# Kernel tuning notes

Hardware: AMD Instinct MI355X
Metric: run time of the kernel (lower is better)

Reference implementation:

```python
import jax, jax.numpy as jnp
from jax import lax
import numpy as np
import math

INPUT_DIM = 64
HIDDEN_DIM = 512
SEQ_LEN = 256
BATCH = 512
PRED_LEN = 24
NUM_TARGETS = 1


def setup_inputs() -> dict:
    key = jax.random.key(0)
    ks = jax.random.split(key, 10)
    stdv = 1.0 / math.sqrt(HIDDEN_DIM)
    u = lambda k, shape: jax.random.uniform(k, shape, jnp.float32, -stdv, stdv)
    return {
        "x": jax.random.normal(ks[0], (BATCH, SEQ_LEN, INPUT_DIM), jnp.float32),
        "Wa": u(ks[1], (INPUT_DIM, INPUT_DIM)),
        "Ua": u(ks[2], (2 * HIDDEN_DIM, INPUT_DIM)),
        "ba": jnp.zeros((INPUT_DIM,), jnp.float32),
        "Va": u(ks[3], (INPUT_DIM, INPUT_DIM)),
        "W_ih": u(ks[4], (4 * HIDDEN_DIM, INPUT_DIM)),
        "W_hh": u(ks[5], (4 * HIDDEN_DIM, HIDDEN_DIM)),
        "b_ih": u(ks[6], (4 * HIDDEN_DIM,)),
        "b_hh": u(ks[7], (4 * HIDDEN_DIM,)),
        "fc_w": u(ks[8], (PRED_LEN * NUM_TARGETS, HIDDEN_DIM)),
        "fc_b": u(ks[9], (PRED_LEN * NUM_TARGETS,)),
    }


def reference(x, Wa, Ua, ba, Va, W_ih, W_hh, b_ih, b_hh, fc_w, fc_b):
    B, S, D = x.shape
    H = W_hh.shape[1]

    def step(carry, x_t):
        h, c = carry  # [B,H] each
        # attention gate over input features
        hc = jnp.concatenate([h, c], axis=1)  # [B,2H]
        a_t = jnp.tanh(x_t @ Wa + hc @ Ua + ba) @ Va  # [B,D]
        alpha_t = jax.nn.softmax(a_t, axis=1)
        x_att = alpha_t * x_t
        # torch.nn.LSTMCell: gates in order i, f, g, o
        gates = x_att @ W_ih.T + h @ W_hh.T + b_ih + b_hh  # [B,4H]
        i, f, g, o = jnp.split(gates, 4, axis=1)
        c_new = jax.nn.sigmoid(f) * c + jax.nn.sigmoid(i) * jnp.tanh(g)
        h_new = jax.nn.sigmoid(o) * jnp.tanh(c_new)
        return (h_new, c_new), None

    h0 = jnp.zeros((B, H), x.dtype)
    c0 = jnp.zeros((B, H), x.dtype)
    (h_T, _), _ = lax.scan(step, (h0, c0), jnp.swapaxes(x, 0, 1))  # scan over seq
    y = h_T @ fc_w.T + fc_b  # [B, pred_len*num_targets]
    return y.reshape(B, PRED_LEN, NUM_TARGETS)
```

## Files before the change

### kernel.cpp

```cpp
#include <hip/hip_runtime.h>
#include <math.h>

#define B 512
#define S 256
#define D 64
#define H 512
#define BH (B*H)

typedef __attribute__((ext_vector_type(8))) short short8;
typedef __attribute__((ext_vector_type(4))) float f32x4;

__device__ inline unsigned short f2bf(float v) {
    unsigned int u = __float_as_uint(v);
    unsigned int r = (u + 0x7fffu + ((u >> 16) & 1u)) >> 16;
    return (unsigned short)r;
}
__device__ inline float bf2f(unsigned short b) {
    return __uint_as_float(((unsigned int)b) << 16);
}

__global__ __launch_bounds__(256) void init_zero(
    float* __restrict__ h32, float* __restrict__ c32,
    unsigned short* __restrict__ hHi, unsigned short* __restrict__ hLo)
{
    int i = blockIdx.x * blockDim.x + threadIdx.x;
    if (i < BH) {
        h32[i] = 0.f;
        c32[i] = 0.f;
        hHi[i] = 0;
        hLo[i] = 0;
    }
}

__global__ __launch_bounds__(256) void prep_weights(
    const float* __restrict__ Whh, const float* __restrict__ Wih,
    unsigned short* __restrict__ wswz)
{
    const int jt = blockIdx.x;
    const int kb = blockIdx.y;
    const int t = threadIdx.x;
    const int jj = t >> 3;
    const int kk8 = t & 7;
    const int jg = jt*32 + jj;
    const int u = jg >> 2, q = jg & 3;
    const int Wrow = q*H + u;

    const float* src = (kb < 8) ? (Whh + (size_t)Wrow*H + kb*64 + kk8*8)
                                : (Wih + (size_t)Wrow*D + kk8*8);
    float v[8];
    *(float4*)&v[0] = *(const float4*)(src);
    *(float4*)&v[4] = *(const float4*)(src + 4);

    unsigned short hi[8], lo[8];
    #pragma unroll
    for (int e = 0; e < 8; ++e) {
        hi[e] = f2bf(v[e]);
        lo[e] = f2bf(v[e] - bf2f(hi[e]));
    }
    const int ks = kk8 >> 2, cg = kk8 & 3;
    const size_t slab = (size_t)(jt*9 + kb) * 4096;
    const size_t oH = slab + (size_t)(0*2048 + ks*1024 + cg*256 + jj*8);
    const size_t oL = slab + (size_t)(1*2048 + ks*1024 + cg*256 + jj*8);
    *(short8*)(wswz + oH) = *(const short8*)hi;
    *(short8*)(wswz + oL) = *(const short8*)lo;
}

__global__ __launch_bounds__(256) void attn_kernel(
    const float* __restrict__ x, const float* __restrict__ Wa,
    const float* __restrict__ Ua, const float* __restrict__ ba,
    const float* __restrict__ Va,
    const float* __restrict__ h32, const float* __restrict__ c32,
    unsigned short* __restrict__ xHi, unsigned short* __restrict__ xLo, int t)
{
    const int d = threadIdx.x & 63;
    const int r = (threadIdx.x >> 6) & 1;
    const int p = threadIdx.x >> 7;
    const int b = blockIdx.x * 2 + r;

    const int rd = t & 1;
    const float* __restrict__ hrow = h32 + (size_t)rd*BH + (size_t)b*H;
    const float* __restrict__ crow = c32 + (size_t)b*H;
    const float* __restrict__ xrow = x + ((size_t)b*S + t)*D;

    __shared__ float part[2][2][64];
    __shared__ float ta[2][64];
    __shared__ float pv[2][2][64];

    float a = 0.f;
    if (p == 0) {
        a = ba[d];
        #pragma unroll 8
        for (int k = 0; k < D; ++k) a += xrow[k] * Wa[k*D + d];
        #pragma unroll 8
        for (int k = 0; k < H; ++k) a += hrow[k] * Ua[k*D + d];
    } else {
        #pragma unroll 8
        for (int k = 0; k < H; ++k) a += crow[k] * Ua[(size_t)(H + k)*D + d];
    }
    part[r][p][d] = a;
    __syncthreads();
    if (p == 0) {
        ta[r][d] = tanhf(part[r][0][d] + part[r][1][d]);
    }
    __syncthreads();
    float av = 0.f;
    {
        const int k0 = p * 32;
        #pragma unroll 8
        for (int k = k0; k < k0 + 32; ++k) av += ta[r][k] * Va[k*D + d];
    }
    pv[r][p][d] = av;
    __syncthreads();
    float v = pv[r][0][d] + pv[r][1][d];
    float m = v;
    #pragma unroll
    for (int o = 32; o > 0; o >>= 1) m = fmaxf(m, __shfl_xor(m, o));
    float e = expf(v - m);
    float ssum = e;
    #pragma unroll
    for (int o = 32; o > 0; o >>= 1) ssum += __shfl_xor(ssum, o);
    if (p == 0) {
        float val = (e / ssum) * xrow[d];
        unsigned short hi = f2bf(val);
        unsigned short lo = f2bf(val - bf2f(hi));
        xHi[(size_t)b*D + d] = hi;
        xLo[(size_t)b*D + d] = lo;
    }
}

__global__ __launch_bounds__(256, 2) void gates_kernel(
    const unsigned short* __restrict__ wswz,
    const unsigned short* __restrict__ hHi, const unsigned short* __restrict__ hLo,
    const unsigned short* __restrict__ xHi, const unsigned short* __restrict__ xLo,
    float* __restrict__ h32, float* __restrict__ c32,
    const float* __restrict__ bih, const float* __restrict__ bhh, int t)
{
    const int tid = threadIdx.x;
    const int lane = tid & 63;
    const int wid = tid >> 6;
    const int wr = wid >> 1, wc = wid & 1;
    const int jt = blockIdx.x;
    const int b0 = blockIdx.y * 64;
    const int l15 = lane & 15;
    const int cg = lane >> 4;

    __shared__ __align__(16) unsigned short aHi[2][64][72];
    __shared__ __align__(16) unsigned short aLo[2][64][72];
    __shared__ float gout[64][37];

    const int rd = t & 1, wrs = rd ^ 1;
    const unsigned short* __restrict__ hHiR = hHi + (size_t)rd*BH;
    const unsigned short* __restrict__ hLoR = hLo + (size_t)rd*BH;

    const int srow = tid >> 2;
    const int q4 = tid & 3;

    {
        const size_t base = (size_t)(b0 + srow)*H + q4*16;
        *(short8*)&aHi[0][srow][q4*16]     = *(const short8*)(hHiR + base);
        *(short8*)&aHi[0][srow][q4*16 + 8] = *(const short8*)(hHiR + base + 8);
        *(short8*)&aLo[0][srow][q4*16]     = *(const short8*)(hLoR + base);
        *(short8*)&aLo[0][srow][q4*16 + 8] = *(const short8*)(hLoR + base + 8);
    }
    __syncthreads();

    f32x4 acc0 = {0,0,0,0}, acc1 = {0,0,0,0};
    const int lofs = cg*256 + (wc*16 + l15)*8;

    for (int kb = 0; kb < 9; ++kb) {
        const int cur = kb & 1;
        const unsigned short* pB = wswz + (size_t)(jt*9 + kb)*4096;
        short8 bh0 = *(const short8*)(pB + 0*2048 + 0*1024 + lofs);
        short8 bh1 = *(const short8*)(pB + 0*2048 + 1*1024 + lofs);
        short8 bl0 = *(const short8*)(pB + 1*2048 + 0*1024 + lofs);
        short8 bl1 = *(const short8*)(pB + 1*2048 + 1*1024 + lofs);
        if (kb < 8) {
            const unsigned short *sh, *sl;
            if (kb + 1 < 8) {
                const size_t base = (size_t)(b0 + srow)*H + (kb + 1)*64 + q4*16;
                sh = hHiR + base; sl = hLoR + base;
            } else {
                const size_t base = (size_t)(b0 + srow)*D + q4*16;
                sh = xHi + base; sl = xLo + base;
            }
            *(short8*)&aHi[cur^1][srow][q4*16]     = *(const short8*)sh;
            *(short8*)&aHi[cur^1][srow][q4*16 + 8] = *(const short8*)(sh + 8);
            *(short8*)&aLo[cur^1][srow][q4*16]     = *(const short8*)sl;
            *(short8*)&aLo[cur^1][srow][q4*16 + 8] = *(const short8*)(sl + 8);
        }
        const int ar = wr*32 + l15;
        short8 ah00 = *(const short8*)&aHi[cur][ar     ][cg*8];
        short8 ah01 = *(const short8*)&aHi[cur][ar     ][32 + cg*8];
        short8 ah10 = *(const short8*)&aHi[cur][ar + 16][cg*8];
        short8 ah11 = *(const short8*)&aHi[cur][ar + 16][32 + cg*8];
        short8 al00 = *(const short8*)&aLo[cur][ar     ][cg*8];
        short8 al01 = *(const short8*)&aLo[cur][ar     ][32 + cg*8];
        short8 al10 = *(const short8*)&aLo[cur][ar + 16][cg*8];
        short8 al11 = *(const short8*)&aLo[cur][ar + 16][32 + cg*8];

        acc0 = __builtin_amdgcn_mfma_f32_16x16x32_bf16(ah00, bh0, acc0, 0,0,0);
        acc1 = __builtin_amdgcn_mfma_f32_16x16x32_bf16(ah10, bh0, acc1, 0,0,0);
        acc0 = __builtin_amdgcn_mfma_f32_16x16x32_bf16(ah00, bl0, acc0, 0,0,0);
        acc1 = __builtin_amdgcn_mfma_f32_16x16x32_bf16(ah10, bl0, acc1, 0,0,0);
        acc0 = __builtin_amdgcn_mfma_f32_16x16x32_bf16(al00, bh0, acc0, 0,0,0);
        acc1 = __builtin_amdgcn_mfma_f32_16x16x32_bf16(al10, bh0, acc1, 0,0,0);
        acc0 = __builtin_amdgcn_mfma_f32_16x16x32_bf16(ah01, bh1, acc0, 0,0,0);
        acc1 = __builtin_amdgcn_mfma_f32_16x16x32_bf16(ah11, bh1, acc1, 0,0,0);
        acc0 = __builtin_amdgcn_mfma_f32_16x16x32_bf16(ah01, bl1, acc0, 0,0,0);
        acc1 = __builtin_amdgcn_mfma_f32_16x16x32_bf16(ah11, bl1, acc1, 0,0,0);
        acc0 = __builtin_amdgcn_mfma_f32_16x16x32_bf16(al01, bh1, acc0, 0,0,0);
        acc1 = __builtin_amdgcn_mfma_f32_16x16x32_bf16(al11, bh1, acc1, 0,0,0);
        __syncthreads();
    }

    {
        const int m0 = cg * 4;
        #pragma unroll
        for (int r = 0; r < 4; ++r) {
            gout[wr*32 + m0 + r     ][wc*16 + l15] = acc0[r];
            gout[wr*32 + 16 + m0 + r][wc*16 + l15] = acc1[r];
        }
    }
    __syncthreads();
    {
        const int u8 = tid & 7;
        const int u_glob = jt*8 + u8;
        const float bs0 = bih[0*H + u_glob] + bhh[0*H + u_glob];
        const float bs1 = bih[1*H + u_glob] + bhh[1*H + u_glob];
        const float bs2 = bih[2*H + u_glob] + bhh[2*H + u_glob];
        const float bs3 = bih[3*H + u_glob] + bhh[3*H + u_glob];
        float* __restrict__ h32w = h32 + (size_t)wrs*BH;
        unsigned short* __restrict__ hHiW = (unsigned short*)hHi + (size_t)wrs*BH;
        unsigned short* __restrict__ hLoW = (unsigned short*)hLo + (size_t)wrs*BH;
        #pragma unroll
        for (int pp = 0; pp < 2; ++pp) {
            const int row_loc = (tid >> 3) + pp*32;
            const int b = b0 + row_loc;
            float gi = gout[row_loc][u8*4 + 0] + bs0;
            float gf = gout[row_loc][u8*4 + 1] + bs1;
            float gg = gout[row_loc][u8*4 + 2] + bs2;
            float go = gout[row_loc][u8*4 + 3] + bs3;
            const size_t idx = (size_t)b*H + u_glob;
            float c_old = c32[idx];
            float si = 1.f/(1.f + expf(-gi));
            float sf = 1.f/(1.f + expf(-gf));
            float so = 1.f/(1.f + expf(-go));
            float cn = sf*c_old + si*tanhf(gg);
            float hn = so*tanhf(cn);
            c32[idx] = cn;
            h32w[idx] = hn;
            unsigned short hi = f2bf(hn);
            unsigned short lo = f2bf(hn - bf2f(hi));
            hHiW[idx] = hi;
            hLoW[idx] = lo;
        }
    }
}

__global__ __launch_bounds__(256) void fc_kernel(
    const float* __restrict__ fcw, const float* __restrict__ fcb,
    const float* __restrict__ h32, float* __restrict__ out)
{
    const int b = blockIdx.x;
    __shared__ float hrow[H];
    const float* __restrict__ hp = h32 + (size_t)b*H;
    for (int k = threadIdx.x; k < H; k += 256) hrow[k] = hp[k];
    __syncthreads();
    int j = threadIdx.x;
    if (j < 24) {
        float a = fcb[j];
        #pragma unroll 8
        for (int k = 0; k < H; ++k) a += hrow[k] * fcw[j*H + k];
        out[b*24 + j] = a;
    }
}

extern "C" void kernel_launch(void* const* d_in, const int* in_sizes, int n_in,
                              void* d_out, int out_size, void* d_ws, size_t ws_size,
                              hipStream_t stream) {
    const float* x   = (const float*)d_in[0];
    const float* Wa  = (const float*)d_in[1];
    const float* Ua  = (const float*)d_in[2];
    const float* ba  = (const float*)d_in[3];
    const float* Va  = (const float*)d_in[4];
    const float* Wih = (const float*)d_in[5];
    const float* Whh = (const float*)d_in[6];
    const float* bih = (const float*)d_in[7];
    const float* bhh = (const float*)d_in[8];
    const float* fcw = (const float*)d_in[9];
    const float* fcb = (const float*)d_in[10];
    float* out = (float*)d_out;

    char* base = (char*)d_ws;
    float* h32 = (float*)(base);
    float* c32 = (float*)(base + (size_t)2*BH*4);
    unsigned short* hHi = (unsigned short*)(base + (size_t)3*BH*4);
    unsigned short* hLo = hHi + (size_t)2*BH;
    unsigned short* xHi = hLo + (size_t)2*BH;
    unsigned short* xLo = xHi + (size_t)B*D;
    unsigned short* wswz = xLo + (size_t)B*D;

    hipLaunchKernelGGL(init_zero, dim3((BH + 255)/256), dim3(256), 0, stream,
                       h32, c32, hHi, hLo);
    hipLaunchKernelGGL(prep_weights, dim3(64, 9), dim3(256), 0, stream,
                       Whh, Wih, wswz);
    for (int t = 0; t < S; ++t) {
        hipLaunchKernelGGL(attn_kernel, dim3(B/2), dim3(256), 0, stream,
                           x, Wa, Ua, ba, Va, h32, c32, xHi, xLo, t);
        hipLaunchKernelGGL(gates_kernel, dim3(64, 8), dim3(256), 0, stream,
                           wswz, hHi, hLo, xHi, xLo, h32, c32, bih, bhh, t);
    }
    hipLaunchKernelGGL(fc_kernel, dim3(B), dim3(256), 0, stream, fcw, fcb, h32, out);
}
```

Before: 8.449 ms.

## Replace per-step kernel launches with persistent cooperative kernel and grid barriers

Fuses the attention and gate kernels for all 256 timesteps into one cooperative persistent kernel of 512 workgroups. Steps are separated by a hierarchical atomic grid barrier instead of 512 separate launches. The aim is to remove launch overhead and inter-kernel gaps. The change also reorganises A-tile staging through registers, using a single LDS buffer with extra syncthreads per k-block. The barrier relies on all workgroups being co-resident and has a spin timeout that could break correctness if exceeded. If the cooperative launch fails, the code falls back to the old launch loop.

```diff
diff --git a/kernel.cpp b/kernel.cpp
--- a/kernel.cpp
+++ b/kernel.cpp
@@ -6,6 +6,7 @@
 #define D 64
 #define H 512
 #define BH (B*H)
+#define NWG 512
 
 typedef __attribute__((ext_vector_type(8))) short short8;
 typedef __attribute__((ext_vector_type(4))) float f32x4;
@@ -17,6 +18,41 @@
 }
 __device__ inline float bf2f(unsigned short b) {
     return __uint_as_float(((unsigned int)b) << 16);
+}
+
+__device__ inline void grid_barrier(unsigned int* bar, int g) {
+    __syncthreads();
+    if (threadIdx.x == 0) {
+        __threadfence();
+        unsigned int myGen = __hip_atomic_load(&bar[576], __ATOMIC_RELAXED,
+                                               __HIP_MEMORY_SCOPE_AGENT);
+        unsigned int a = __hip_atomic_fetch_add(&bar[(g & 7)*64], 1u,
+                             __ATOMIC_ACQ_REL, __HIP_MEMORY_SCOPE_AGENT);
+        bool done_bump = false;
+        if (a == 63u) {
+            __hip_atomic_store(&bar[(g & 7)*64], 0u, __ATOMIC_RELAXED,
+                               __HIP_MEMORY_SCOPE_AGENT);
+            unsigned int d = __hip_atomic_fetch_add(&bar[512], 1u,
+                                 __ATOMIC_ACQ_REL, __HIP_MEMORY_SCOPE_AGENT);
+            if (d == 7u) {
+                __hip_atomic_store(&bar[512], 0u, __ATOMIC_RELAXED,
+                                   __HIP_MEMORY_SCOPE_AGENT);
+                __hip_atomic_store(&bar[576], myGen + 1u, __ATOMIC_RELEASE,
+                                   __HIP_MEMORY_SCOPE_AGENT);
+                done_bump = true;
+            }
+        }
+        if (!done_bump) {
+            unsigned int spin = 0;
+            while (__hip_atomic_load(&bar[576], __ATOMIC_RELAXED,
+                                     __HIP_MEMORY_SCOPE_AGENT) == myGen) {
+                __builtin_amdgcn_s_sleep(2);
+                if (++spin > (1u << 22)) break;
+            }
+        }
+        __threadfence();
+    }
+    __syncthreads();
 }
 
 __global__ __launch_bounds__(256) void init_zero(
@@ -24,12 +60,7 @@
     unsigned short* __restrict__ hHi, unsigned short* __restrict__ hLo)
 {
     int i = blockIdx.x * blockDim.x + threadIdx.x;
-    if (i < BH) {
-        h32[i] = 0.f;
-        c32[i] = 0.f;
-        hHi[i] = 0;
-        hLo[i] = 0;
-    }
+    if (i < BH) { h32[i] = 0.f; c32[i] = 0.f; hHi[i] = 0; hLo[i] = 0; }
 }
 
 __global__ __launch_bounds__(256) void prep_weights(
@@ -57,12 +88,10 @@
         hi[e] = f2bf(v[e]);
         lo[e] = f2bf(v[e] - bf2f(hi[e]));
     }
-    const int ks = kk8 >> 2, cg = kk8 & 3;
+    const int ks = kk8 >> 2, cg2 = kk8 & 3;
     const size_t slab = (size_t)(jt*9 + kb) * 4096;
-    const size_t oH = slab + (size_t)(0*2048 + ks*1024 + cg*256 + jj*8);
-    const size_t oL = slab + (size_t)(1*2048 + ks*1024 + cg*256 + jj*8);
-    *(short8*)(wswz + oH) = *(const short8*)hi;
-    *(short8*)(wswz + oL) = *(const short8*)lo;
+    *(short8*)(wswz + slab + (size_t)(0*2048 + ks*1024 + cg2*256 + jj*8)) = *(const short8*)hi;
+    *(short8*)(wswz + slab + (size_t)(1*2048 + ks*1024 + cg2*256 + jj*8)) = *(const short8*)lo;
 }
 
 __global__ __launch_bounds__(256) void attn_kernel(
@@ -99,9 +128,7 @@
     }
     part[r][p][d] = a;
     __syncthreads();
-    if (p == 0) {
-        ta[r][d] = tanhf(part[r][0][d] + part[r][1][d]);
-    }
+    if (p == 0) ta[r][d] = tanhf(part[r][0][d] + part[r][1][d]);
     __syncthreads();
     float av = 0.f;
     {
@@ -142,7 +169,7 @@
     const int jt = blockIdx.x;
     const int b0 = blockIdx.y * 64;
     const int l15 = lane & 15;
-    const int cg = lane >> 4;
+    const int cgi = lane >> 4;
 
     __shared__ __align__(16) unsigned short aHi[2][64][72];
     __shared__ __align__(16) unsigned short aLo[2][64][72];
@@ -165,7 +192,7 @@
     __syncthreads();
 
     f32x4 acc0 = {0,0,0,0}, acc1 = {0,0,0,0};
-    const int lofs = cg*256 + (wc*16 + l15)*8;
+    const int lofs = cgi*256 + (wc*16 + l15)*8;
 
     for (int kb = 0; kb < 9; ++kb) {
         const int cur = kb & 1;
@@ -189,14 +216,14 @@
             *(short8*)&aLo[cur^1][srow][q4*16 + 8] = *(const short8*)(sl + 8);
         }
         const int ar = wr*32 + l15;
-        short8 ah00 = *(const short8*)&aHi[cur][ar     ][cg*8];
-        short8 ah01 = *(const short8*)&aHi[cur][ar     ][32 + cg*8];
-        short8 ah10 = *(const short8*)&aHi[cur][ar + 16][cg*8];
-        short8 ah11 = *(const short8*)&aHi[cur][ar + 16][32 + cg*8];
-        short8 al00 = *(const short8*)&aLo[cur][ar     ][cg*8];
-        short8 al01 = *(const short8*)&aLo[cur][ar     ][32 + cg*8];
-        short8 al10 = *(const short8*)&aLo[cur][ar + 16][cg*8];
-        short8 al11 = *(const short8*)&aLo[cur][ar + 16][32 + cg*8];
+        short8 ah00 = *(const short8*)&aHi[cur][ar     ][cgi*8];
+        short8 ah01 = *(const short8*)&aHi[cur][ar     ][32 + cgi*8];
+        short8 ah10 = *(const short8*)&aHi[cur][ar + 16][cgi*8];
+        short8 ah11 = *(const short8*)&aHi[cur][ar + 16][32 + cgi*8];
+        short8 al00 = *(const short8*)&aLo[cur][ar     ][cgi*8];
+        short8 al01 = *(const short8*)&aLo[cur][ar     ][32 + cgi*8];
+        short8 al10 = *(const short8*)&aLo[cur][ar + 16][cgi*8];
+        short8 al11 = *(const short8*)&aLo[cur][ar + 16][32 + cgi*8];
 
         acc0 = __builtin_amdgcn_mfma_f32_16x16x32_bf16(ah00, bh0, acc0, 0,0,0);
         acc1 = __builtin_amdgcn_mfma_f32_16x16x32_bf16(ah10, bh0, acc1, 0,0,0);
@@ -214,7 +241,7 @@
     }
 
     {
-        const int m0 = cg * 4;
+        const int m0 = cgi * 4;
         #pragma unroll
         for (int r = 0; r < 4; ++r) {
             gout[wr*32 + m0 + r     ][wc*16 + l15] = acc0[r];
@@ -257,6 +284,211 @@
     }
 }
 
+__global__ __launch_bounds__(256, 2) void persist_kernel(
+    const float* __restrict__ x, const float* __restrict__ Wa,
+    const float* __restrict__ Ua, const float* __restrict__ ba,
+    const float* __restrict__ Va,
+    const unsigned short* __restrict__ wswz,
+    unsigned short* __restrict__ hHi, unsigned short* __restrict__ hLo,
+    unsigned short* __restrict__ xHi, unsigned short* __restrict__ xLo,
+    float* __restrict__ h32, float* __restrict__ c32,
+    const float* __restrict__ bih, const float* __restrict__ bhh,
+    unsigned int* bar)
+{
+    const int g = blockIdx.x;
+    const int tid = threadIdx.x;
+    const int lane = tid & 63;
+
+    __shared__ __align__(16) unsigned short aHi[64][72];
+    __shared__ __align__(16) unsigned short aLo[64][72];
+    __shared__ float gout[64][37];
+    float* arena = &gout[0][0];
+
+    for (int i = g*256 + tid; i < BH; i += NWG*256) {
+        h32[i] = 0.f; c32[i] = 0.f; hHi[i] = 0; hLo[i] = 0;
+    }
+    grid_barrier(bar, g);
+
+    const int jt = g & 63;
+    const int rt = g >> 6;
+    const int b0g = rt * 64;
+    const int wid = tid >> 6;
+    const int wr = wid >> 1, wc = wid & 1;
+    const int l15 = lane & 15;
+    const int cgi = lane >> 4;
+    const int srow = tid >> 2;
+    const int q4 = tid & 3;
+    const int lofs = cgi*256 + (wc*16 + l15)*8;
+
+    const int a_d = tid & 63;
+    const int a_r = (tid >> 6) & 1;
+    const int a_p = tid >> 7;
+    const int a_b = g*2 + a_r;
+
+    for (int t = 0; t < S; ++t) {
+        const int rd = t & 1, wrs = rd ^ 1;
+        const unsigned short* __restrict__ hHiR = hHi + (size_t)rd*BH;
+        const unsigned short* __restrict__ hLoR = hLo + (size_t)rd*BH;
+
+        if (g < 256) {
+            const float* __restrict__ hrow = h32 + (size_t)rd*BH + (size_t)a_b*H;
+            const float* __restrict__ crow = c32 + (size_t)a_b*H;
+            const float* __restrict__ xrow = x + ((size_t)a_b*S + t)*D;
+
+            float a = 0.f;
+            if (a_p == 0) {
+                a = ba[a_d];
+                #pragma unroll 8
+                for (int k = 0; k < D; ++k) a += xrow[k] * Wa[k*D + a_d];
+                #pragma unroll 8
+                for (int k = 0; k < H; ++k) a += hrow[k] * Ua[k*D + a_d];
+            } else {
+                #pragma unroll 8
+                for (int k = 0; k < H; ++k) a += crow[k] * Ua[(size_t)(H + k)*D + a_d];
+            }
+            arena[a_r*128 + a_p*64 + a_d] = a;
+            __syncthreads();
+            if (a_p == 0) {
+                float pre = arena[a_r*128 + a_d] + arena[a_r*128 + 64 + a_d];
+                arena[256 + a_r*64 + a_d] = tanhf(pre);
+            }
+            __syncthreads();
+            float av = 0.f;
+            {
+                const int k0 = a_p * 32;
+                #pragma unroll 8
+                for (int k = k0; k < k0 + 32; ++k)
+                    av += arena[256 + a_r*64 + k] * Va[k*D + a_d];
+            }
+            arena[384 + a_r*128 + a_p*64 + a_d] = av;
+            __syncthreads();
+            float v = arena[384 + a_r*128 + a_d] + arena[384 + a_r*128 + 64 + a_d];
+            float m = v;
+            #pragma unroll
+            for (int o = 32; o > 0; o >>= 1) m = fmaxf(m, __shfl_xor(m, o));
+            float e = expf(v - m);
+            float ssum = e;
+            #pragma unroll
+            for (int o = 32; o > 0; o >>= 1) ssum += __shfl_xor(ssum, o);
+            if (a_p == 0) {
+                float val = (e / ssum) * xrow[a_d];
+                unsigned short hi = f2bf(val);
+                unsigned short lo = f2bf(val - bf2f(hi));
+                xHi[(size_t)a_b*D + a_d] = hi;
+                xLo[(size_t)a_b*D + a_d] = lo;
+            }
+            __syncthreads();
+        }
+
+        short8 lh0, lh1, ll0, ll1;
+        {
+            const size_t base = (size_t)(b0g + srow)*H + q4*16;
+            lh0 = *(const short8*)(hHiR + base);
+            lh1 = *(const short8*)(hHiR + base + 8);
+            ll0 = *(const short8*)(hLoR + base);
+            ll1 = *(const short8*)(hLoR + base + 8);
+        }
+
+        grid_barrier(bar, g);
+
+        f32x4 acc0 = {0,0,0,0}, acc1 = {0,0,0,0};
+
+        for (int kb = 0; kb < 9; ++kb) {
+            __syncthreads();
+            *(short8*)&aHi[srow][q4*16]     = lh0;
+            *(short8*)&aHi[srow][q4*16 + 8] = lh1;
+            *(short8*)&aLo[srow][q4*16]     = ll0;
+            *(short8*)&aLo[srow][q4*16 + 8] = ll1;
+            __syncthreads();
+            if (kb < 8) {
+                const unsigned short *sh, *sl;
+                if (kb + 1 < 8) {
+                    const size_t base = (size_t)(b0g + srow)*H + (kb + 1)*64 + q4*16;
+                    sh = hHiR + base; sl = hLoR + base;
+                } else {
+                    const size_t base = (size_t)(b0g + srow)*D + q4*16;
+                    sh = xHi + base; sl = xLo + base;
+                }
+                lh0 = *(const short8*)sh; lh1 = *(const short8*)(sh + 8);
+                ll0 = *(const short8*)sl; ll1 = *(const short8*)(sl + 8);
+            }
+            const unsigned short* pB = wswz + (size_t)(jt*9 + kb)*4096;
+            short8 bh0 = *(const short8*)(pB + 0*2048 + 0*1024 + lofs);
+            short8 bh1 = *(const short8*)(pB + 0*2048 + 1*1024 + lofs);
+            short8 bl0 = *(const short8*)(pB + 1*2048 + 0*1024 + lofs);
+            short8 bl1 = *(const short8*)(pB + 1*2048 + 1*1024 + lofs);
+
+            const int ar = wr*32 + l15;
+            short8 ah00 = *(const short8*)&aHi[ar     ][cgi*8];
+            short8 ah01 = *(const short8*)&aHi[ar     ][32 + cgi*8];
+            short8 ah10 = *(const short8*)&aHi[ar + 16][cgi*8];
+            short8 ah11 = *(const short8*)&aHi[ar + 16][32 + cgi*8];
+            short8 al00 = *(const short8*)&aLo[ar     ][cgi*8];
+            short8 al01 = *(const short8*)&aLo[ar     ][32 + cgi*8];
+            short8 al10 = *(const short8*)&aLo[ar + 16][cgi*8];
+            short8 al11 = *(const short8*)&aLo[ar + 16][32 + cgi*8];
+
+            acc0 = __builtin_amdgcn_mfma_f32_16x16x32_bf16(ah00, bh0, acc0, 0,0,0);
+            acc1 = __builtin_amdgcn_mfma_f32_16x16x32_bf16(ah10, bh0, acc1, 0,0,0);
+            acc0 = __builtin_amdgcn_mfma_f32_16x16x32_bf16(ah00, bl0, acc0, 0,0,0);
+            acc1 = __builtin_amdgcn_mfma_f32_16x16x32_bf16(ah10, bl0, acc1, 0,0,0);
+            acc0 = __builtin_amdgcn_mfma_f32_16x16x32_bf16(al00, bh0, acc0, 0,0,0);
+            acc1 = __builtin_amdgcn_mfma_f32_16x16x32_bf16(al10, bh0, acc1, 0,0,0);
+            acc0 = __builtin_amdgcn_mfma_f32_16x16x32_bf16(ah01, bh1, acc0, 0,0,0);
+            acc1 = __builtin_amdgcn_mfma_f32_16x16x32_bf16(ah11, bh1, acc1, 0,0,0);
+            acc0 = __builtin_amdgcn_mfma_f32_16x16x32_bf16(ah01, bl1, acc0, 0,0,0);
+            acc1 = __builtin_amdgcn_mfma_f32_16x16x32_bf16(ah11, bl1, acc1, 0,0,0);
+            acc0 = __builtin_amdgcn_mfma_f32_16x16x32_bf16(al01, bh1, acc0, 0,0,0);
+            acc1 = __builtin_amdgcn_mfma_f32_16x16x32_bf16(al11, bh1, acc1, 0,0,0);
+        }
+        __syncthreads();
+
+        {
+            const int m0 = cgi * 4;
+            #pragma unroll
+            for (int r = 0; r < 4; ++r) {
+                gout[wr*32 + m0 + r     ][wc*16 + l15] = acc0[r];
+                gout[wr*32 + 16 + m0 + r][wc*16 + l15] = acc1[r];
+            }
+        }
+        __syncthreads();
+        {
+            const int u8 = tid & 7;
+            const int u_glob = jt*8 + u8;
+            const float bs0 = bih[0*H + u_glob] + bhh[0*H + u_glob];
+            const float bs1 = bih[1*H + u_glob] + bhh[1*H + u_glob];
+            const float bs2 = bih[2*H + u_glob] + bhh[2*H + u_glob];
+            const float bs3 = bih[3*H + u_glob] + bhh[3*H + u_glob];
+            float* __restrict__ h32w = h32 + (size_t)wrs*BH;
+            unsigned short* __restrict__ hHiW = hHi + (size_t)wrs*BH;
+            unsigned short* __restrict__ hLoW = hLo + (size_t)wrs*BH;
+            #pragma unroll
+            for (int pp = 0; pp < 2; ++pp) {
+                const int row_loc = (tid >> 3) + pp*32;
+                const int b = b0g + row_loc;
+                float gi = gout[row_loc][u8*4 + 0] + bs0;
+                float gf = gout[row_loc][u8*4 + 1] + bs1;
+                float ggt = gout[row_loc][u8*4 + 2] + bs2;
+                float go = gout[row_loc][u8*4 + 3] + bs3;
+                const size_t idx = (size_t)b*H + u_glob;
+                float c_old = c32[idx];
+                float si = 1.f/(1.f + expf(-gi));
+                float sf = 1.f/(1.f + expf(-gf));
+                float so = 1.f/(1.f + expf(-go));
+                float cn = sf*c_old + si*tanhf(ggt);
+                float hn = so*tanhf(cn);
+                c32[idx] = cn;
+                h32w[idx] = hn;
+                unsigned short hi = f2bf(hn);
+                unsigned short lo = f2bf(hn - bf2f(hi));
+                hHiW[idx] = hi;
+                hLoW[idx] = lo;
+            }
+        }
+        grid_barrier(bar, g);
+    }
+}
+
 __global__ __launch_bounds__(256) void fc_kernel(
     const float* __restrict__ fcw, const float* __restrict__ fcb,
     const float* __restrict__ h32, float* __restrict__ out)
@@ -299,16 +531,35 @@
     unsigned short* xHi = hLo + (size_t)2*BH;
     unsigned short* xLo = xHi + (size_t)B*D;
     unsigned short* wswz = xLo + (size_t)B*D;
-
-    hipLaunchKernelGGL(init_zero, dim3((BH + 255)/256), dim3(256), 0, stream,
-                       h32, c32, hHi, hLo);
+    unsigned int* bar = (unsigned int*)(wswz + (size_t)576*4096);
+
+    hipMemsetAsync(bar, 0, 4096, stream);
     hipLaunchKernelGGL(prep_weights, dim3(64, 9), dim3(256), 0, stream,
                        Whh, Wih, wswz);
-    for (int t = 0; t < S; ++t) {
-        hipLaunchKernelGGL(attn_kernel, dim3(B/2), dim3(256), 0, stream,
-                           x, Wa, Ua, ba, Va, h32, c32, xHi, xLo, t);
-        hipLaunchKernelGGL(gates_kernel, dim3(64, 8), dim3(256), 0, stream,
-                           wswz, hHi, hLo, xHi, xLo, h32, c32, bih, bhh, t);
+
+    int maxBlk = 0;
+    hipError_t oe = hipOccupancyMaxActiveBlocksPerMultiprocessor(
+        &maxBlk, persist_kernel, 256, 0);
+    bool coop = (oe == hipSuccess && maxBlk >= 2);
+    if (coop) {
+        void* args[] = {
+            (void*)&x, (void*)&Wa, (void*)&Ua, (void*)&ba, (void*)&Va,
+            (void*)&wswz, (void*)&hHi, (void*)&hLo, (void*)&xHi, (void*)&xLo,
+            (void*)&h32, (void*)&c32, (void*)&bih, (void*)&bhh, (void*)&bar
+        };
+        hipError_t rc = hipLaunchCooperativeKernel((void*)persist_kernel,
+                            dim3(NWG), dim3(256), args, 0, stream);
+        if (rc != hipSuccess) coop = false;
+    }
+    if (!coop) {
+        hipLaunchKernelGGL(init_zero, dim3((BH + 255)/256), dim3(256), 0, stream,
+                           h32, c32, hHi, hLo);
+        for (int t = 0; t < S; ++t) {
+            hipLaunchKernelGGL(attn_kernel, dim3(B/2), dim3(256), 0, stream,
+                               x, Wa, Ua, ba, Va, h32, c32, xHi, xLo, t);
+            hipLaunchKernelGGL(gates_kernel, dim3(64, 8), dim3(256), 0, stream,
+                               wswz, hHi, hLo, xHi, xLo, h32, c32, bih, bhh, t);
+        }
     }
     hipLaunchKernelGGL(fc_kernel, dim3(B), dim3(256), 0, stream, fcw, fcb, h32, out);
 }
```

After: 8.529 ms. About the same (+1.0%).
